# Kernel optimization log

Measured on AMD Instinct MI355X. Metric: run time of the kernel, lower is better.

The kernel has to match this reference:

```python
import jax, jax.numpy as jnp
import numpy as np

B, CIN, H, W = 4, 1024, 64, 64
PLANES = 256
K = 3
DIL = 2
PAD = DIL * (K - 1) // 2  # = 2
EPS = 1e-5


def setup_inputs() -> dict:
    key = jax.random.key(0)
    ks = jax.random.split(key, 16)
    d = {}
    d['x'] = jax.random.normal(ks[0], (B, CIN, H, W), dtype=jnp.float32)
    # conv1: 1x1, inplanes->planes, no bias
    d['w1'] = jax.random.normal(ks[1], (PLANES, CIN), dtype=jnp.float32) * 0.02
    d['gamma1'] = jnp.ones((PLANES,), jnp.float32)
    d['beta1'] = jnp.zeros((PLANES,), jnp.float32)
    d['mean1'] = jax.random.normal(ks[2], (PLANES,), dtype=jnp.float32) * 0.1
    d['var1'] = jax.random.uniform(ks[3], (PLANES,), minval=0.5, maxval=1.5, dtype=jnp.float32)
    # deform_offset: 3x3 conv planes->18, with bias
    d['woff'] = jax.random.normal(ks[4], (18, PLANES, K, K), dtype=jnp.float32) * 0.01
    d['boff'] = jnp.zeros((18,), jnp.float32)
    # conv2 (deformable): 3x3 planes->planes, with bias
    d['w2'] = jax.random.normal(ks[5], (PLANES, PLANES, K, K), dtype=jnp.float32) * 0.02
    d['bconv2'] = jnp.zeros((PLANES,), jnp.float32)
    d['gamma2'] = jnp.ones((PLANES,), jnp.float32)
    d['beta2'] = jnp.zeros((PLANES,), jnp.float32)
    d['mean2'] = jax.random.normal(ks[6], (PLANES,), dtype=jnp.float32) * 0.1
    d['var2'] = jax.random.uniform(ks[7], (PLANES,), minval=0.5, maxval=1.5, dtype=jnp.float32)
    # conv3: 1x1 planes->planes*4, no bias
    d['w3'] = jax.random.normal(ks[8], (PLANES * 4, PLANES), dtype=jnp.float32) * 0.02
    d['gamma3'] = jnp.ones((PLANES * 4,), jnp.float32)
    d['beta3'] = jnp.zeros((PLANES * 4,), jnp.float32)
    d['mean3'] = jax.random.normal(ks[9], (PLANES * 4,), dtype=jnp.float32) * 0.1
    d['var3'] = jax.random.uniform(ks[10], (PLANES * 4,), minval=0.5, maxval=1.5, dtype=jnp.float32)
    return d


def _bn(x, gamma, beta, mean, var):
    # inference-mode BatchNorm over channel dim (NCHW)
    inv = jax.lax.rsqrt(var + EPS)
    return (x - mean[:, None, None]) * (inv * gamma)[:, None, None] + beta[:, None, None]


def _deform_conv(x, offset, w, b):
    # x: [B,C,H,W]; offset: [B,18,H,W] ordered (dy,dx) per kernel tap; w: [O,C,3,3]
    Bn, C, Hh, Ww = x.shape
    off = offset.reshape(Bn, K * K, 2, Hh, Ww)
    off_y, off_x = off[:, :, 0], off[:, :, 1]          # [B,9,H,W]
    kk = jnp.arange(K * K)
    base_y = (kk // K) * DIL - PAD                      # [9]
    base_x = (kk % K) * DIL - PAD
    ys = jnp.arange(Hh, dtype=x.dtype)
    xs = jnp.arange(Ww, dtype=x.dtype)
    py = base_y.astype(x.dtype)[None, :, None, None] + ys[None, None, :, None] + off_y
    px = base_x.astype(x.dtype)[None, :, None, None] + xs[None, None, None, :] + off_x

    def sample_one(img, py1, px1):
        # img [C,H,W]; py1/px1 [9,H,W] -> [C,9,H,W] bilinear with zero padding
        y0 = jnp.floor(py1)
        x0 = jnp.floor(px1)
        wy = py1 - y0
        wx = px1 - x0

        def gather(yc, xc):
            yi = yc.astype(jnp.int32)
            xi = xc.astype(jnp.int32)
            valid = ((yi >= 0) & (yi < Hh) & (xi >= 0) & (xi < Ww)).astype(img.dtype)
            yi = jnp.clip(yi, 0, Hh - 1)
            xi = jnp.clip(xi, 0, Ww - 1)
            return img[:, yi, xi] * valid[None]

        v00 = gather(y0, x0)
        v01 = gather(y0, x0 + 1)
        v10 = gather(y0 + 1, x0)
        v11 = gather(y0 + 1, x0 + 1)
        return (v00 * ((1 - wy) * (1 - wx))[None] + v01 * ((1 - wy) * wx)[None]
                + v10 * (wy * (1 - wx))[None] + v11 * (wy * wx)[None])

    sampled = jax.vmap(sample_one)(x, py, px)           # [B,C,9,H,W]
    out = jnp.einsum('bckhw,ock->bohw', sampled, w.reshape(w.shape[0], C, K * K))
    return out + b[None, :, None, None]


def reference(x, w1, gamma1, beta1, mean1, var1, woff, boff, w2, bconv2,
              gamma2, beta2, mean2, var2, w3, gamma3, beta3, mean3, var3):
    residual = x
    out = jnp.einsum('bchw,oc->bohw', x, w1)            # conv1 1x1
    out = jax.nn.relu(_bn(out, gamma1, beta1, mean1, var1))
    offset = jax.lax.conv_general_dilated(
        out, woff, window_strides=(1, 1), padding=((PAD, PAD), (PAD, PAD)),
        rhs_dilation=(DIL, DIL), dimension_numbers=('NCHW', 'OIHW', 'NCHW'))
    offset = offset + boff[None, :, None, None]
    out = _deform_conv(out, offset, w2, bconv2)
    out = jax.nn.relu(_bn(out, gamma2, beta2, mean2, var2))
    out = jnp.einsum('bchw,oc->bohw', out, w3)          # conv3 1x1
    out = _bn(out, gamma3, beta3, mean3, var3)
    return jax.nn.relu(out + residual)
```

## Files before the change

### kernel.cpp

```cpp
#include <hip/hip_runtime.h>

#define EPS_BN 1e-5f

typedef __bf16 bf16x8 __attribute__((ext_vector_type(8)));
typedef float f32x4 __attribute__((ext_vector_type(4)));

__device__ __forceinline__ unsigned short f2bf(float f) {
  union { float f; unsigned u; } v; v.f = f;
  unsigned r = v.u + 0x7fffu + ((v.u >> 16) & 1u);
  return (unsigned short)(r >> 16);
}
__device__ __forceinline__ float bf2f(unsigned short h) {
  union { unsigned u; float f; } v; v.u = ((unsigned)h) << 16;
  return v.f;
}

__global__ void cvt_bf16(const float* __restrict__ in, unsigned short* __restrict__ out, int n) {
  int i = blockIdx.x * 256 + threadIdx.x;
  if (i < n) out[i] = f2bf(in[i]);
}

__global__ void zero16(uint4* __restrict__ p, int n16) {
  int i = blockIdx.x * 256 + threadIdx.x;
  if (i < n16) p[i] = uint4{0, 0, 0, 0};
}

__global__ void reorder_w2(const float* __restrict__ w2, unsigned short* __restrict__ w2r) {
  int i = blockIdx.x * 256 + threadIdx.x;
  int o = i / 2304, r = i % 2304;
  int kk = r / 256, c = r % 256;
  w2r[i] = f2bf(w2[(size_t)o * 2304 + c * 9 + kk]);
}

__global__ void reorder_woff(const float* __restrict__ woff, unsigned short* __restrict__ wob) {
  int i = blockIdx.x * 256 + threadIdx.x;
  if (i >= 32 * 2304) return;
  int o = i / 2304, r = i % 2304;
  int kk = r / 256, c = r % 256;
  wob[i] = (o < 18) ? f2bf(woff[(size_t)o * 2304 + c * 9 + kk]) : (unsigned short)0;
}

__global__ void prep_bn(const float* g1, const float* b1, const float* m1, const float* v1,
                        const float* g2, const float* b2, const float* m2, const float* v2,
                        const float* bconv2, float* s1, float* h1, float* s2, float* h2) {
  int c = threadIdx.x;
  float sc1 = rsqrtf(v1[c] + EPS_BN) * g1[c];
  s1[c] = sc1; h1[c] = b1[c] - m1[c] * sc1;
  float sc2 = rsqrtf(v2[c] + EPS_BN) * g2[c];
  s2[c] = sc2; h2[c] = b2[c] + (bconv2[c] - m2[c]) * sc2;
}

__global__ __launch_bounds__(256) void transpose_x(const float* __restrict__ x,
                                                   unsigned short* __restrict__ xT) {
  __shared__ float t[32][33];
  int b = blockIdx.z;
  int p0 = blockIdx.x * 32, c0 = blockIdx.y * 32;
  int tx = threadIdx.x & 31, ty = threadIdx.x >> 5;
  const float* xb = x + (size_t)b * 1024 * 4096;
#pragma unroll
  for (int j = 0; j < 4; ++j) {
    int c = c0 + ty + j * 8;
    t[ty + j * 8][tx] = xb[(size_t)c * 4096 + p0 + tx];
  }
  __syncthreads();
  unsigned short* xTb = xT + (size_t)b * 4096 * 1024;
#pragma unroll
  for (int j = 0; j < 4; ++j) {
    int p = p0 + ty + j * 8;
    xTb[(size_t)p * 1024 + c0 + tx] = f2bf(t[tx][ty + j * 8]);
  }
}

__global__ __launch_bounds__(256) void gemm_split(
    const unsigned short* __restrict__ A, const unsigned short* __restrict__ Bm,
    float* __restrict__ part, int M, int N, int K, int KH) {
  __shared__ unsigned short sA[128 * 32];
  __shared__ unsigned short sB[128 * 32];
  int tid = threadIdx.x, lane = tid & 63, wv = tid >> 6;
  int z = blockIdx.z;
  int m0 = blockIdx.y * 128, n0 = blockIdx.x * 128;
  f32x4 acc[4][4] = {};
  int rowA = tid >> 2;
  int kcol = (tid & 3) * 8;
  int wm = wv & 1, wn = wv >> 1;
  int lane15 = lane & 15, quad8 = (lane >> 4) * 8;
  int kend = z * KH + KH;

  for (int k0 = z * KH; k0 < kend; k0 += 32) {
    __syncthreads();
#pragma unroll
    for (int r = 0; r < 2; ++r) {
      const unsigned short* gp = A + (size_t)(m0 + r * 64 + rowA) * K + k0 + kcol;
      __builtin_amdgcn_global_load_lds((const __attribute__((address_space(1))) void*)gp,
                                       (__attribute__((address_space(3))) void*)&sA[r * 2048 + wv * 512],
                                       16, 0, 0);
    }
#pragma unroll
    for (int r = 0; r < 2; ++r) {
      const unsigned short* gp = Bm + (size_t)(n0 + r * 64 + rowA) * K + k0 + kcol;
      __builtin_amdgcn_global_load_lds((const __attribute__((address_space(1))) void*)gp,
                                       (__attribute__((address_space(3))) void*)&sB[r * 2048 + wv * 512],
                                       16, 0, 0);
    }
    __syncthreads();
    bf16x8 afr[4], bfr[4];
#pragma unroll
    for (int mi = 0; mi < 4; ++mi)
      afr[mi] = *(const bf16x8*)&sA[(wm * 64 + mi * 16 + lane15) * 32 + quad8];
#pragma unroll
    for (int ni = 0; ni < 4; ++ni)
      bfr[ni] = *(const bf16x8*)&sB[(wn * 64 + ni * 16 + lane15) * 32 + quad8];
#pragma unroll
    for (int mi = 0; mi < 4; ++mi)
#pragma unroll
      for (int ni = 0; ni < 4; ++ni)
        acc[mi][ni] = __builtin_amdgcn_mfma_f32_16x16x32_bf16(afr[mi], bfr[ni], acc[mi][ni], 0, 0, 0);
  }

  float* outF = part + (size_t)z * M * N;
#pragma unroll
  for (int mi = 0; mi < 4; ++mi) {
#pragma unroll
    for (int ni = 0; ni < 4; ++ni) {
      int col = n0 + wn * 64 + ni * 16 + lane15;
#pragma unroll
      for (int reg = 0; reg < 4; ++reg) {
        int row = m0 + wm * 64 + mi * 16 + (lane >> 4) * 4 + reg;
        outF[(size_t)row * N + col] = acc[mi][ni][reg];
      }
    }
  }
}

template <int PAD>
__global__ __launch_bounds__(256) void epi_bn(const float* __restrict__ part,
                                              const float* __restrict__ scale,
                                              const float* __restrict__ shift,
                                              unsigned short* __restrict__ outT,
                                              unsigned short* __restrict__ outP) {
  int gid = blockIdx.x * 256 + threadIdx.x;
  int row = gid >> 5, c0 = (gid & 31) * 8;
  const float* a = part + (size_t)row * 256 + c0;
  const float* b = a + (size_t)16384 * 256;
  float va[8], vb[8], sc[8], sh[8];
  *(float4*)&va[0] = *(const float4*)a;       *(float4*)&va[4] = *(const float4*)(a + 4);
  *(float4*)&vb[0] = *(const float4*)b;       *(float4*)&vb[4] = *(const float4*)(b + 4);
  *(float4*)&sc[0] = *(const float4*)(scale + c0); *(float4*)&sc[4] = *(const float4*)(scale + c0 + 4);
  *(float4*)&sh[0] = *(const float4*)(shift + c0); *(float4*)&sh[4] = *(const float4*)(shift + c0 + 4);
  unsigned o[4];
#pragma unroll
  for (int j = 0; j < 4; ++j) {
    float lo = fmaxf((va[2 * j] + vb[2 * j]) * sc[2 * j] + sh[2 * j], 0.f);
    float hi = fmaxf((va[2 * j + 1] + vb[2 * j + 1]) * sc[2 * j + 1] + sh[2 * j + 1], 0.f);
    o[j] = (unsigned)f2bf(lo) | ((unsigned)f2bf(hi) << 16);
  }
  uint4 pk{o[0], o[1], o[2], o[3]};
  *(uint4*)(outT + (size_t)row * 256 + c0) = pk;
  if constexpr (PAD) {
    int bb = row >> 12, p = row & 4095;
    *(uint4*)(outP + (((size_t)(bb * 68) + (p >> 6) + 2) * 68 + (p & 63) + 2) * 256 + c0) = pk;
  }
}

__global__ __launch_bounds__(256) void gemm_res(
    const unsigned short* __restrict__ A, const unsigned short* __restrict__ Bm,
    float* __restrict__ outp, const float* __restrict__ gamma, const float* __restrict__ beta,
    const float* __restrict__ mean, const float* __restrict__ var,
    const float* __restrict__ resid, int M, int N, int K, long bStrideB, long bStrideOut) {
  __shared__ unsigned short sA[128 * 32];
  __shared__ unsigned short sB[128 * 32];
  int tid = threadIdx.x, lane = tid & 63, wv = tid >> 6;
  int z = blockIdx.z;
  const unsigned short* Bz = Bm + (size_t)z * bStrideB;
  int m0 = blockIdx.y * 128, n0 = blockIdx.x * 128;
  f32x4 acc[4][4] = {};
  int rowA = tid >> 2;
  int kcol = (tid & 3) * 8;
  int wm = wv & 1, wn = wv >> 1;
  int lane15 = lane & 15, quad8 = (lane >> 4) * 8;

  for (int k0 = 0; k0 < K; k0 += 32) {
    __syncthreads();
#pragma unroll
    for (int r = 0; r < 2; ++r) {
      const unsigned short* gp = A + (size_t)(m0 + r * 64 + rowA) * K + k0 + kcol;
      __builtin_amdgcn_global_load_lds((const __attribute__((address_space(1))) void*)gp,
                                       (__attribute__((address_space(3))) void*)&sA[r * 2048 + wv * 512],
                                       16, 0, 0);
    }
#pragma unroll
    for (int r = 0; r < 2; ++r) {
      const unsigned short* gp = Bz + (size_t)(n0 + r * 64 + rowA) * K + k0 + kcol;
      __builtin_amdgcn_global_load_lds((const __attribute__((address_space(1))) void*)gp,
                                       (__attribute__((address_space(3))) void*)&sB[r * 2048 + wv * 512],
                                       16, 0, 0);
    }
    __syncthreads();
    bf16x8 afr[4], bfr[4];
#pragma unroll
    for (int mi = 0; mi < 4; ++mi)
      afr[mi] = *(const bf16x8*)&sA[(wm * 64 + mi * 16 + lane15) * 32 + quad8];
#pragma unroll
    for (int ni = 0; ni < 4; ++ni)
      bfr[ni] = *(const bf16x8*)&sB[(wn * 64 + ni * 16 + lane15) * 32 + quad8];
#pragma unroll
    for (int mi = 0; mi < 4; ++mi)
#pragma unroll
      for (int ni = 0; ni < 4; ++ni)
        acc[mi][ni] = __builtin_amdgcn_mfma_f32_16x16x32_bf16(afr[mi], bfr[ni], acc[mi][ni], 0, 0, 0);
  }

  float* outF = outp + (size_t)z * bStrideOut;
  const float* res = resid + (size_t)z * bStrideOut;
#pragma unroll
  for (int mi = 0; mi < 4; ++mi) {
#pragma unroll
    for (int ni = 0; ni < 4; ++ni) {
      int col = n0 + wn * 64 + ni * 16 + lane15;
#pragma unroll
      for (int reg = 0; reg < 4; ++reg) {
        int row = m0 + wm * 64 + mi * 16 + (lane >> 4) * 4 + reg;
        int ch = row;
        float inv = rsqrtf(var[ch] + EPS_BN) * gamma[ch];
        float v = (acc[mi][ni][reg] - mean[ch]) * inv + beta[ch];
        v += res[(size_t)row * N + col];
        outF[(size_t)row * N + col] = fmaxf(v, 0.f);
      }
    }
  }
}

__global__ __launch_bounds__(256) void off_gemm(const unsigned short* __restrict__ actP,
                                                const unsigned short* __restrict__ wob,
                                                const float* __restrict__ boff,
                                                float* __restrict__ offsP) {
  __shared__ unsigned short sA[64 * 64];
  __shared__ unsigned short sB[32 * 64];
  int tid = threadIdx.x, lane = tid & 63, wv = tid >> 6;
  int m0 = blockIdx.x * 64;
  int lane15 = lane & 15, quad8 = (lane >> 4) * 8;
  int rowA = tid >> 3;
  int kc = (tid & 7) * 8;

  const unsigned short* baseA[2];
#pragma unroll
  for (int r = 0; r < 2; ++r) {
    int row = m0 + r * 32 + rowA;
    int b = row >> 12, p = row & 4095;
    baseA[r] = actP + (((size_t)(b * 68) + (p >> 6) + 2) * 68 + (p & 63) + 2) * 256 + kc;
  }
  const unsigned short* baseB = wob + (size_t)rowA * 2304 + kc;

  f32x4 acc[2] = {};
  for (int kk = 0; kk < 9; ++kk) {
    int shift = ((kk / 3) * 2 - 2) * 68 + ((kk % 3) * 2 - 2);
#pragma unroll 1
    for (int c0 = 0; c0 < 256; c0 += 64) {
      __syncthreads();
#pragma unroll
      for (int r = 0; r < 2; ++r) {
        const unsigned short* gp = baseA[r] + (long)shift * 256 + c0;
        __builtin_amdgcn_global_load_lds((const __attribute__((address_space(1))) void*)gp,
                                         (__attribute__((address_space(3))) void*)&sA[r * 2048 + wv * 512],
                                         16, 0, 0);
      }
      {
        const unsigned short* gp = baseB + kk * 256 + c0;
        __builtin_amdgcn_global_load_lds((const __attribute__((address_space(1))) void*)gp,
                                         (__attribute__((address_space(3))) void*)&sB[wv * 512],
                                         16, 0, 0);
      }
      __syncthreads();
      bf16x8 afr[2], bfr[2][2];
#pragma unroll
      for (int kq = 0; kq < 2; ++kq) {
        afr[kq] = *(const bf16x8*)&sA[(wv * 16 + lane15) * 64 + kq * 32 + quad8];
#pragma unroll
        for (int ni = 0; ni < 2; ++ni)
          bfr[kq][ni] = *(const bf16x8*)&sB[(ni * 16 + lane15) * 64 + kq * 32 + quad8];
      }
#pragma unroll
      for (int kq = 0; kq < 2; ++kq)
#pragma unroll
        for (int ni = 0; ni < 2; ++ni)
          acc[ni] = __builtin_amdgcn_mfma_f32_16x16x32_bf16(afr[kq], bfr[kq][ni], acc[ni], 0, 0, 0);
    }
  }

#pragma unroll
  for (int ni = 0; ni < 2; ++ni) {
    int o = ni * 16 + lane15;
    if (o < 18) {
      float bo = boff[o];
#pragma unroll
      for (int reg = 0; reg < 4; ++reg) {
        int row = m0 + wv * 16 + (lane >> 4) * 4 + reg;
        offsP[(size_t)row * 18 + o] = acc[ni][reg] + bo;
      }
    }
  }
}

__global__ __launch_bounds__(256) void deform_sample(const unsigned short* __restrict__ act1T,
                                                     const float* __restrict__ offsP,
                                                     unsigned short* __restrict__ S) {
  int g = threadIdx.x >> 5, t = threadIdx.x & 31;
  int idx = blockIdx.x * 8 + g;
  int b = idx >> 12, p = idx & 4095;
  int h = p >> 6, w = p & 63;
  const unsigned short* actb = act1T + (size_t)b * 4096 * 256 + t * 8;
  unsigned short* Sp = S + (size_t)idx * 2304 + t * 8;
  float ov = (t < 18) ? offsP[(size_t)idx * 18 + t] : 0.f;
#pragma unroll
  for (int kk = 0; kk < 9; ++kk) {
    float offy = __shfl(ov, 2 * kk, 32);
    float offx = __shfl(ov, 2 * kk + 1, 32);
    float py = (float)(h + (kk / 3) * 2 - 2) + offy;
    float px = (float)(w + (kk % 3) * 2 - 2) + offx;
    float fy = floorf(py), fx = floorf(px);
    int y0 = (int)fy, x0 = (int)fx;
    float wy = py - fy, wx = px - fx;
    bool yv0 = (y0 >= 0 && y0 < 64), yv1 = (y0 >= -1 && y0 < 63);
    bool xv0 = (x0 >= 0 && x0 < 64), xv1 = (x0 >= -1 && x0 < 63);
    const unsigned short* cb = actb + (y0 * 64 + x0) * 256;
    uint4 q00{0,0,0,0}, q01{0,0,0,0}, q10{0,0,0,0}, q11{0,0,0,0};
    if (yv0 && xv0) q00 = *(const uint4*)(cb);
    if (yv0 && xv1) q01 = *(const uint4*)(cb + 256);
    if (yv1 && xv0) q10 = *(const uint4*)(cb + 64 * 256);
    if (yv1 && xv1) q11 = *(const uint4*)(cb + 64 * 256 + 256);
    float w00 = (1.f - wy) * (1.f - wx), w01 = (1.f - wy) * wx;
    float w10 = wy * (1.f - wx), w11 = wy * wx;
    unsigned u00[4] = {q00.x, q00.y, q00.z, q00.w};
    unsigned u01[4] = {q01.x, q01.y, q01.z, q01.w};
    unsigned u10[4] = {q10.x, q10.y, q10.z, q10.w};
    unsigned u11[4] = {q11.x, q11.y, q11.z, q11.w};
    unsigned out[4];
#pragma unroll
    for (int j = 0; j < 4; ++j) {
      float lo = bf2f((unsigned short)(u00[j] & 0xffffu)) * w00 +
                 bf2f((unsigned short)(u01[j] & 0xffffu)) * w01 +
                 bf2f((unsigned short)(u10[j] & 0xffffu)) * w10 +
                 bf2f((unsigned short)(u11[j] & 0xffffu)) * w11;
      float hi = bf2f((unsigned short)(u00[j] >> 16)) * w00 +
                 bf2f((unsigned short)(u01[j] >> 16)) * w01 +
                 bf2f((unsigned short)(u10[j] >> 16)) * w10 +
                 bf2f((unsigned short)(u11[j] >> 16)) * w11;
      out[j] = (unsigned)f2bf(lo) | ((unsigned)f2bf(hi) << 16);
    }
    *(uint4*)(Sp + kk * 256) = uint4{out[0], out[1], out[2], out[3]};
  }
}

extern "C" void kernel_launch(void* const* d_in, const int* in_sizes, int n_in,
                              void* d_out, int out_size, void* d_ws, size_t ws_size,
                              hipStream_t stream) {
  const float* x      = (const float*)d_in[0];
  const float* w1     = (const float*)d_in[1];
  const float* gamma1 = (const float*)d_in[2];
  const float* beta1  = (const float*)d_in[3];
  const float* mean1  = (const float*)d_in[4];
  const float* var1   = (const float*)d_in[5];
  const float* woff   = (const float*)d_in[6];
  const float* boff   = (const float*)d_in[7];
  const float* w2     = (const float*)d_in[8];
  const float* bconv2 = (const float*)d_in[9];
  const float* gamma2 = (const float*)d_in[10];
  const float* beta2  = (const float*)d_in[11];
  const float* mean2  = (const float*)d_in[12];
  const float* var2   = (const float*)d_in[13];
  const float* w3     = (const float*)d_in[14];
  const float* gamma3 = (const float*)d_in[15];
  const float* beta3  = (const float*)d_in[16];
  const float* mean3  = (const float*)d_in[17];
  const float* var3   = (const float*)d_in[18];

  char* ws = (char*)d_ws;
  unsigned short* xT    = (unsigned short*)(ws);
  unsigned short* act1T = (unsigned short*)(ws + 33554432);
  unsigned short* act2T = (unsigned short*)(ws + 41943040);
  unsigned short* S     = (unsigned short*)(ws + 50331648);
  float*          offs  = (float*)(ws + 125829120);
  unsigned short* w1b   = (unsigned short*)(ws + 127008768);
  unsigned short* w2r   = (unsigned short*)(ws + 127533056);
  unsigned short* w3b   = (unsigned short*)(ws + 128712704);
  float*          bnS1  = (float*)(ws + 129236992);
  float*          bnH1  = (float*)(ws + 129238016);
  float*          bnS2  = (float*)(ws + 129239040);
  float*          bnH2  = (float*)(ws + 129240064);
  unsigned short* act1P = S;
  float*          part1 = (float*)(ws + 62914560);
  float*          part2 = (float*)ws;
  unsigned short* wob   = xT;

  cvt_bf16<<<1024, 256, 0, stream>>>(w1, w1b, 262144);
  cvt_bf16<<<1024, 256, 0, stream>>>(w3, w3b, 262144);
  reorder_w2<<<2304, 256, 0, stream>>>(w2, w2r);
  zero16<<<2312, 256, 0, stream>>>((uint4*)act1P, 591872);
  prep_bn<<<1, 256, 0, stream>>>(gamma1, beta1, mean1, var1, gamma2, beta2, mean2, var2,
                                 bconv2, bnS1, bnH1, bnS2, bnH2);
  transpose_x<<<dim3(128, 32, 4), 256, 0, stream>>>(x, xT);

  gemm_split<<<dim3(2, 128, 2), 256, 0, stream>>>(xT, w1b, part1, 16384, 256, 1024, 512);
  epi_bn<1><<<2048, 256, 0, stream>>>(part1, bnS1, bnH1, act1T, act1P);

  reorder_woff<<<288, 256, 0, stream>>>(woff, wob);
  off_gemm<<<256, 256, 0, stream>>>(act1P, wob, boff, offs);
  deform_sample<<<dim3(2048), 256, 0, stream>>>(act1T, offs, S);

  gemm_split<<<dim3(2, 128, 2), 256, 0, stream>>>(S, w2r, part2, 16384, 256, 2304, 1152);
  epi_bn<0><<<2048, 256, 0, stream>>>(part2, bnS2, bnH2, act2T, nullptr);

  gemm_res<<<dim3(32, 8, 4), 256, 0, stream>>>(w3b, act2T, (float*)d_out, gamma3, beta3, mean3,
                                               var3, x, 1024, 4096, 256, 4096L * 256, 4194304L);
}
```

Baseline: 322.4 us.

## Fold BN3 scale into w3 and coalesce gemm_res epilogue via LDS staging

The BN3 scale is folded into the bf16 w3 weights up front, and a precomputed per-channel shift replaces the per-element rsqrt and four parameter loads in the final GEMM epilogue. The accumulator tile is staged through shared memory so the residual reads and output writes become row-contiguous float4 accesses instead of scattered scalar ones. This adds two small prep kernels, extra barriers and shared memory in gemm_res, and rounds the scaled weights to bf16 slightly differently.

```diff
diff --git a/kernel.cpp b/kernel.cpp
--- a/kernel.cpp
+++ b/kernel.cpp
@@ -48,6 +48,21 @@
   s1[c] = sc1; h1[c] = b1[c] - m1[c] * sc1;
   float sc2 = rsqrtf(v2[c] + EPS_BN) * g2[c];
   s2[c] = sc2; h2[c] = b2[c] + (bconv2[c] - m2[c]) * sc2;
+}
+
+__global__ void prep_bn3(const float* __restrict__ g, const float* __restrict__ b,
+                         const float* __restrict__ m, const float* __restrict__ v,
+                         float* __restrict__ scale, float* __restrict__ shift) {
+  int c = blockIdx.x * 256 + threadIdx.x;
+  float sc = rsqrtf(v[c] + EPS_BN) * g[c];
+  scale[c] = sc;
+  shift[c] = b[c] - m[c] * sc;
+}
+
+__global__ void cvt_w3s(const float* __restrict__ w3, const float* __restrict__ scale,
+                        unsigned short* __restrict__ out) {
+  int i = blockIdx.x * 256 + threadIdx.x;
+  out[i] = f2bf(w3[i] * scale[i >> 8]);
 }
 
 __global__ __launch_bounds__(256) void transpose_x(const float* __restrict__ x,
@@ -164,11 +179,11 @@
 
 __global__ __launch_bounds__(256) void gemm_res(
     const unsigned short* __restrict__ A, const unsigned short* __restrict__ Bm,
-    float* __restrict__ outp, const float* __restrict__ gamma, const float* __restrict__ beta,
-    const float* __restrict__ mean, const float* __restrict__ var,
+    float* __restrict__ outp, const float* __restrict__ shift3,
     const float* __restrict__ resid, int M, int N, int K, long bStrideB, long bStrideOut) {
   __shared__ unsigned short sA[128 * 32];
   __shared__ unsigned short sB[128 * 32];
+  __shared__ float tbuf[32 * 132];
   int tid = threadIdx.x, lane = tid & 63, wv = tid >> 6;
   int z = blockIdx.z;
   const unsigned short* Bz = Bm + (size_t)z * bStrideB;
@@ -177,7 +192,7 @@
   int rowA = tid >> 2;
   int kcol = (tid & 3) * 8;
   int wm = wv & 1, wn = wv >> 1;
-  int lane15 = lane & 15, quad8 = (lane >> 4) * 8;
+  int lane15 = lane & 15, quad8 = (lane >> 4) * 8, quad = lane >> 4;
 
   for (int k0 = 0; k0 < K; k0 += 32) {
     __syncthreads();
@@ -212,20 +227,33 @@
 
   float* outF = outp + (size_t)z * bStrideOut;
   const float* res = resid + (size_t)z * bStrideOut;
+  int trow = tid >> 3;
+  int tcol = (tid & 7) * 4;
+  int growBase = m0 + (trow >> 4) * 64 + (trow & 15);
 #pragma unroll
   for (int mi = 0; mi < 4; ++mi) {
-#pragma unroll
-    for (int ni = 0; ni < 4; ++ni) {
-      int col = n0 + wn * 64 + ni * 16 + lane15;
-#pragma unroll
-      for (int reg = 0; reg < 4; ++reg) {
-        int row = m0 + wm * 64 + mi * 16 + (lane >> 4) * 4 + reg;
-        int ch = row;
-        float inv = rsqrtf(var[ch] + EPS_BN) * gamma[ch];
-        float v = (acc[mi][ni][reg] - mean[ch]) * inv + beta[ch];
-        v += res[(size_t)row * N + col];
-        outF[(size_t)row * N + col] = fmaxf(v, 0.f);
-      }
+    __syncthreads();
+#pragma unroll
+    for (int ni = 0; ni < 4; ++ni)
+#pragma unroll
+      for (int reg = 0; reg < 4; ++reg)
+        tbuf[(wm * 16 + quad * 4 + reg) * 132 + wn * 64 + ni * 16 + lane15] = acc[mi][ni][reg];
+    __syncthreads();
+    int gr = growBase + mi * 16;
+    float sh = shift3[gr];
+    const float* rp = res + (size_t)gr * N + n0 + tcol;
+    float* op = outF + (size_t)gr * N + n0 + tcol;
+    const float* lp = &tbuf[trow * 132 + tcol];
+#pragma unroll
+    for (int j = 0; j < 4; ++j) {
+      float4 rv = *(const float4*)(rp + j * 32);
+      float4 lv = *(const float4*)(lp + j * 32);
+      float4 ov;
+      ov.x = fmaxf(lv.x + sh + rv.x, 0.f);
+      ov.y = fmaxf(lv.y + sh + rv.y, 0.f);
+      ov.z = fmaxf(lv.z + sh + rv.z, 0.f);
+      ov.w = fmaxf(lv.w + sh + rv.w, 0.f);
+      *(float4*)(op + j * 32) = ov;
     }
   }
 }
@@ -391,9 +419,10 @@
   float*          part1 = (float*)(ws + 62914560);
   float*          part2 = (float*)ws;
   unsigned short* wob   = xT;
+  float*          scale3 = (float*)(ws + 125829120);
+  float*          shift3 = (float*)(ws + 125833216);
 
   cvt_bf16<<<1024, 256, 0, stream>>>(w1, w1b, 262144);
-  cvt_bf16<<<1024, 256, 0, stream>>>(w3, w3b, 262144);
   reorder_w2<<<2304, 256, 0, stream>>>(w2, w2r);
   zero16<<<2312, 256, 0, stream>>>((uint4*)act1P, 591872);
   prep_bn<<<1, 256, 0, stream>>>(gamma1, beta1, mean1, var1, gamma2, beta2, mean2, var2,
@@ -407,9 +436,12 @@
   off_gemm<<<256, 256, 0, stream>>>(act1P, wob, boff, offs);
   deform_sample<<<dim3(2048), 256, 0, stream>>>(act1T, offs, S);
 
+  prep_bn3<<<4, 256, 0, stream>>>(gamma3, beta3, mean3, var3, scale3, shift3);
+  cvt_w3s<<<1024, 256, 0, stream>>>(w3, scale3, w3b);
+
   gemm_split<<<dim3(2, 128, 2), 256, 0, stream>>>(S, w2r, part2, 16384, 256, 2304, 1152);
   epi_bn<0><<<2048, 256, 0, stream>>>(part2, bnS2, bnH2, act2T, nullptr);
 
-  gemm_res<<<dim3(32, 8, 4), 256, 0, stream>>>(w3b, act2T, (float*)d_out, gamma3, beta3, mean3,
-                                               var3, x, 1024, 4096, 256, 4096L * 256, 4194304L);
-}
+  gemm_res<<<dim3(32, 8, 4), 256, 0, stream>>>(w3b, act2T, (float*)d_out, shift3, x,
+                                               1024, 4096, 256, 4096L * 256, 4194304L);
+}
```

Result: no change. 316.5 us (-1.8%).
